# Kernel tuning notes

Measured on AMD Instinct MI355X. Metric: run time of the kernel, lower is better.

## Reference

```python
import jax, jax.numpy as jnp
import numpy as np

B, CIN, COUT, H, W, K, LATENT = 16, 512, 512, 64, 64, 3, 512
SQRT2 = float(np.sqrt(2.0))


def setup_inputs() -> dict:
    key = jax.random.key(0)
    ks = jax.random.split(key, 6)
    return {
        "x": jax.random.normal(ks[0], (B, CIN, H, W), jnp.float32),
        "latent": jax.random.normal(ks[1], (B, LATENT), jnp.float32),
        "noise": jax.random.normal(ks[2], (B, 1, H, W), jnp.float32),
        "affine_weight": jax.random.normal(ks[3], (CIN, LATENT), jnp.float32),
        "affine_bias": jnp.ones((CIN,), jnp.float32),
        "conv_weight": jax.random.normal(ks[4], (COUT, CIN, K, K), jnp.float32),
        "noise_weight": jax.random.normal(ks[5], (), jnp.float32),
        "bias": jnp.zeros((1, COUT, 1, 1), jnp.float32),
    }


def reference(x, latent, noise, affine_weight, affine_bias, conv_weight, noise_weight, bias):
    # NoiseInjection (applied before conv, as in the source)
    x = x + noise_weight * noise

    # AffineNetwork / EqualLinear: w * sqrt(1/in), leaky_relu(.,0.2)*sqrt(2)
    wmul = 1.0 / jnp.sqrt(jnp.float32(affine_weight.shape[1]))
    style = latent @ (affine_weight * wmul).T + affine_bias[None, :]
    style = jax.nn.leaky_relu(style, 0.2) * SQRT2  # [B, Cin]

    # Per-sample modulation (source overwrites the fan-in multiplier; raw weight used)
    w = conv_weight[None] * style[:, None, :, None, None]  # [B, Cout, Cin, kh, kw]
    demod = jax.lax.rsqrt(jnp.sum(w * w, axis=(2, 3, 4), keepdims=True) + 1e-8)
    w = w * demod

    def conv1(xi, wi):  # xi: [Cin,H,W], wi: [Cout,Cin,kh,kw]
        return jax.lax.conv_general_dilated(
            xi[None], wi, (1, 1), "SAME",
            dimension_numbers=("NCHW", "OIHW", "NCHW"))[0]

    out = jax.vmap(conv1)(x, w)  # [B, Cout, H, W]
    return jax.nn.leaky_relu(out + bias, 0.2) * SQRT2
```

## Files before the change

kernel.cpp:

```cpp
#include <hip/hip_runtime.h>

#define SQRT2F 1.41421356237309515f

typedef __attribute__((ext_vector_type(8))) short short8;
typedef __attribute__((ext_vector_type(4))) float floatx4;

static __device__ __forceinline__ unsigned short f2bf(float f) {
    unsigned int u = __float_as_uint(f);
    u += 0x7fffu + ((u >> 16) & 1u);
    return (unsigned short)(u >> 16);
}

static __device__ __forceinline__ void gl_lds16(const void* g, void* l) {
    __builtin_amdgcn_global_load_lds(
        (const __attribute__((address_space(1))) unsigned int*)g,
        (__attribute__((address_space(3))) unsigned int*)l, 16, 0, 0);
}

__global__ void style_kernel(const float* __restrict__ latent,
                             const float* __restrict__ aw,
                             const float* __restrict__ abias,
                             float* __restrict__ style) {
    const int b = blockIdx.x;
    const int t = threadIdx.x;
    const int c = blockIdx.y * 256 + t;
    __shared__ float lat[512];
    lat[t]       = latent[b * 512 + t];
    lat[t + 256] = latent[b * 512 + t + 256];
    __syncthreads();
    const float* row = aw + (size_t)c * 512;
    float s0 = 0.f, s1 = 0.f, s2 = 0.f, s3 = 0.f;
    #pragma unroll 4
    for (int k = 0; k < 512; k += 4) {
        floatx4 r = *(const floatx4*)(row + k);
        s0 += lat[k]     * r[0];
        s1 += lat[k + 1] * r[1];
        s2 += lat[k + 2] * r[2];
        s3 += lat[k + 3] * r[3];
    }
    float s = (s0 + s1) + (s2 + s3);
    s = s * 0.04419417382415922f + abias[c];
    s = (s > 0.f ? s : 0.2f * s) * SQRT2F;
    style[b * 512 + c] = s;
}

__global__ void wprep_kernel(const float* __restrict__ cw,
                             const float* __restrict__ style,
                             unsigned short* __restrict__ wbf,
                             float* __restrict__ demod) {
    const int co = blockIdx.x;
    const int t = threadIdx.x;
    __shared__ float raw[4608];
    __shared__ float sty2[8192];
    __shared__ float r2[512];
    const float* row = cw + (size_t)co * 4608;
    for (int i = t; i < 1152; i += 256)
        ((floatx4*)raw)[i] = ((const floatx4*)row)[i];
    for (int i = t; i < 2048; i += 256) {
        floatx4 v = ((const floatx4*)style)[i];
        ((floatx4*)sty2)[i] = v * v;
    }
    __syncthreads();
    for (int cin = t; cin < 512; cin += 256) {
        float s = 0.f;
        #pragma unroll
        for (int tap = 0; tap < 9; ++tap) { float v = raw[cin * 9 + tap]; s += v * v; }
        r2[cin] = s;
    }
    for (int j = t; j < 576; j += 256) {
        int st = j >> 2, chunk = j & 3;
        int slab = st / 9, tap = st - slab * 9;
        int cb = slab * 32 + chunk * 8;
        short8 o;
        #pragma unroll
        for (int k = 0; k < 8; ++k) o[k] = (short)f2bf(raw[(cb + k) * 9 + tap]);
        *(short8*)(wbf + ((size_t)st * 512 + co) * 32 + chunk * 8) = o;
    }
    __syncthreads();
    const int lane = t & 63, wv = t >> 6;
    #pragma unroll
    for (int bb = 0; bb < 4; ++bb) {
        int b = wv * 4 + bb;
        float s = 0.f;
        for (int cin = lane; cin < 512; cin += 64) s += r2[cin] * sty2[b * 512 + cin];
        #pragma unroll
        for (int off = 32; off > 0; off >>= 1) s += __shfl_down(s, off, 64);
        if (lane == 0) demod[b * 512 + co] = rsqrtf(s + 1e-8f);
    }
}

__global__ void xprep_kernel(const float* __restrict__ x,
                             const float* __restrict__ noise,
                             const float* __restrict__ nwp,
                             const float* __restrict__ style,
                             unsigned short* __restrict__ xp) {
    const int h = blockIdx.x, slab = blockIdx.y, b = blockIdx.z;
    const int t = threadIdx.x;
    __shared__ float tile[32][65];
    const float nw = nwp[0];
    const int w4 = (t & 15) * 4, rh = t >> 4;
    floatx4 nz = *(const floatx4*)(noise + (size_t)b * 4096 + h * 64 + w4);
    #pragma unroll
    for (int p = 0; p < 2; ++p) {
        int cl = p * 16 + rh;
        int cin = slab * 32 + cl;
        floatx4 v = *(const floatx4*)(x + ((size_t)(b * 512 + cin)) * 4096 + h * 64 + w4);
        float sv = style[b * 512 + cin];
        #pragma unroll
        for (int j = 0; j < 4; ++j) tile[cl][w4 + j] = (v[j] + nw * nz[j]) * sv;
    }
    __syncthreads();
    unsigned short* base = xp + ((size_t)(b * 16 + slab) * 4356) * 32;
    const int w2 = t >> 2, chunk = t & 3;
    short8 o;
    #pragma unroll
    for (int j = 0; j < 8; ++j) o[j] = (short)f2bf(tile[chunk * 8 + j][w2]);
    *(short8*)(base + ((size_t)(h + 1) * 66 + (w2 + 1)) * 32 + chunk * 8) = o;
    short8 z = {};
    if (t < 8) {
        int col = (t >> 2) * 65;
        *(short8*)(base + ((size_t)(h + 1) * 66 + col) * 32 + (t & 3) * 8) = z;
    }
    if (h == 0) {
        for (int i = t; i < 264; i += 256)
            *(short8*)(base + (size_t)(i >> 2) * 32 + (i & 3) * 8) = z;
    } else if (h == 63) {
        for (int i = t; i < 264; i += 256)
            *(short8*)(base + ((size_t)65 * 66 + (i >> 2)) * 32 + (i & 3) * 8) = z;
    }
}

__launch_bounds__(256, 2)
__global__ void conv_kernel(const unsigned short* __restrict__ xp,
                            const unsigned short* __restrict__ wbf,
                            const float* __restrict__ demod,
                            const float* __restrict__ bias,
                            float* __restrict__ out) {
    const int b   = blockIdx.z;
    const int co0 = blockIdx.y * 128;
    const int tr  = blockIdx.x >> 2, tc = blockIdx.x & 3;
    const int h0  = tr * 8, w0 = tc * 16;
    const int tid  = threadIdx.x;
    const int lane = tid & 63, wv = tid >> 6;
    const int wr = wv >> 1, wc = wv & 1;
    const int quad = lane >> 4, l16 = lane & 15;

    __shared__ __align__(16) unsigned short lds_x[2][6144];
    __shared__ __align__(16) unsigned short lds_w[2][12288];

    floatx4 acc[4][4] = {};

    int wso[6];
    #pragma unroll
    for (int it = 0; it < 6; ++it) {
        int co = (it * 64 + (tid >> 2)) & 127;
        int lchunk = (tid & 3) ^ ((co >> 1) & 3);
        wso[it] = (it >> 1) * 32768 + co * 64 + lchunk * 16;
    }
    int xo[3];
    #pragma unroll
    for (int it = 0; it < 3; ++it) {
        int pos = it * 64 + (tid >> 2);
        if (pos > 179) pos = 179;
        int r = pos / 18, c = pos - r * 18;
        int lchunk = (tid & 3) ^ ((pos >> 1) & 3);
        xo[it] = (r * 66 + c) * 64 + lchunk * 16;
    }
    const int wvb = wv * 1024;

    int a_off[4];
    #pragma unroll
    for (int mi = 0; mi < 4; ++mi) {
        int co = wr * 64 + mi * 16 + l16;
        a_off[mi] = co * 32 + (quad ^ ((co >> 1) & 3)) * 8;
    }
    int bo2[6][3];
    #pragma unroll
    for (int r = 0; r < 6; ++r)
        #pragma unroll
        for (int c = 0; c < 3; ++c) {
            int pos = (wc * 4 + r) * 18 + c + l16;
            bo2[r][c] = pos * 32 + (quad ^ ((pos >> 1) & 3)) * 8;
        }

    const char* xpb = (const char*)xp + ((size_t)b * 16 * 4356 + h0 * 66 + w0) * 64;
    const char* wb0 = (const char*)wbf + (size_t)co0 * 64;

    #pragma unroll
    for (int it = 0; it < 3; ++it)
        gl_lds16(xpb + xo[it], (char*)lds_x[0] + it * 4096 + wvb);
    #pragma unroll
    for (int it = 0; it < 6; ++it)
        gl_lds16(wb0 + wso[it], (char*)lds_w[0] + it * 4096 + wvb);

    for (int s = 0; s < 16; ++s) {
        short8 xf[6][3];
        #pragma unroll
        for (int g = 0; g < 3; ++g) {
            __syncthreads();
            if (g < 2) {
                const char* gw = wb0 + s * 294912 + (g + 1) * 98304;
                char* lw = (char*)lds_w[(s + g + 1) & 1];
                #pragma unroll
                for (int it = 0; it < 6; ++it)
                    gl_lds16(gw + wso[it], lw + it * 4096 + wvb);
            } else if (s < 15) {
                const char* gw = wb0 + (s + 1) * 294912;
                char* lw = (char*)lds_w[(s + 1) & 1];
                #pragma unroll
                for (int it = 0; it < 6; ++it)
                    gl_lds16(gw + wso[it], lw + it * 4096 + wvb);
            }
            if (g == 0 && s < 15) {
                const char* gx = xpb + (size_t)(s + 1) * 278784;
                char* lx = (char*)lds_x[(s + 1) & 1];
                #pragma unroll
                for (int it = 0; it < 3; ++it)
                    gl_lds16(gx + xo[it], lx + it * 4096 + wvb);
            }
            const unsigned short* wbuf = lds_w[(s + g) & 1];
            const unsigned short* xbuf = lds_x[s & 1];
            if (g == 0) {
                #pragma unroll
                for (int r = 0; r < 4; ++r)
                    #pragma unroll
                    for (int c = 0; c < 3; ++c)
                        xf[r][c] = *(const short8*)(xbuf + bo2[r][c]);
            } else {
                #pragma unroll
                for (int c = 0; c < 3; ++c)
                    xf[g + 3][c] = *(const short8*)(xbuf + bo2[g + 3][c]);
            }
            #pragma unroll
            for (int tl = 0; tl < 3; ++tl) {
                short8 a[4];
                #pragma unroll
                for (int mi = 0; mi < 4; ++mi)
                    a[mi] = *(const short8*)(wbuf + tl * 4096 + a_off[mi]);
                __builtin_amdgcn_s_setprio(1);
                #pragma unroll
                for (int mi = 0; mi < 4; ++mi)
                    #pragma unroll
                    for (int ni = 0; ni < 4; ++ni)
                        acc[mi][ni] = __builtin_amdgcn_mfma_f32_16x16x32_bf16(
                            a[mi], xf[ni + g][tl], acc[mi][ni], 0, 0, 0);
                __builtin_amdgcn_s_setprio(0);
            }
        }
    }

    const float* dmb = demod + b * 512;
    #pragma unroll
    for (int mi = 0; mi < 4; ++mi) {
        const int cob = co0 + wr * 64 + mi * 16 + quad * 4;
        float bv[4], dv[4];
        #pragma unroll
        for (int i = 0; i < 4; ++i) { bv[i] = bias[cob + i]; dv[i] = dmb[cob + i]; }
        #pragma unroll
        for (int ni = 0; ni < 4; ++ni) {
            const int gh = h0 + wc * 4 + ni;
            const int gw = w0 + l16;
            #pragma unroll
            for (int i = 0; i < 4; ++i) {
                float v = acc[mi][ni][i] * dv[i] + bv[i];
                v = (v > 0.f ? v : 0.2f * v) * SQRT2F;
                out[(((size_t)b * 512 + cob + i) * 64 + gh) * 64 + gw] = v;
            }
        }
    }
}

extern "C" void kernel_launch(void* const* d_in, const int* in_sizes, int n_in,
                              void* d_out, int out_size, void* d_ws, size_t ws_size,
                              hipStream_t stream) {
    const float* x      = (const float*)d_in[0];
    const float* latent = (const float*)d_in[1];
    const float* noise  = (const float*)d_in[2];
    const float* aw     = (const float*)d_in[3];
    const float* abias  = (const float*)d_in[4];
    const float* cw     = (const float*)d_in[5];
    const float* nwp    = (const float*)d_in[6];
    const float* bias   = (const float*)d_in[7];
    float* out = (float*)d_out;

    float* style         = (float*)d_ws;
    float* demod         = (float*)((char*)d_ws + 32768);
    unsigned short* wbf  = (unsigned short*)((char*)d_ws + 65536);
    unsigned short* xp   = (unsigned short*)((char*)d_ws + 65536 + 4718592);

    style_kernel<<<dim3(16, 2), dim3(256), 0, stream>>>(latent, aw, abias, style);
    wprep_kernel<<<dim3(512), dim3(256), 0, stream>>>(cw, style, wbf, demod);
    xprep_kernel<<<dim3(64, 16, 16), dim3(256), 0, stream>>>(x, noise, nwp, style, xp);
    conv_kernel<<<dim3(32, 4, 16), dim3(256), 0, stream>>>(xp, wbf, demod, bias, out);
}
```

Measured before the change: 501.0 us.

## Load conv weight fragments directly from global memory instead of staging in LDS

Weight A-fragments are now read straight from global memory into registers for each tap, and the LDS weight double-buffer and its async global-to-LDS copies are removed. Only the input tile is still staged through LDS, so there is one barrier per channel stage instead of three. This frees LDS and cuts barrier and LDS traffic. In exchange, each MFMA group now waits on global or L2 loads with little prefetch, and weights are re-read by both column waves.

```diff
diff --git a/kernel.cpp b/kernel.cpp
--- a/kernel.cpp
+++ b/kernel.cpp
@@ -146,17 +146,9 @@
     const int quad = lane >> 4, l16 = lane & 15;
 
     __shared__ __align__(16) unsigned short lds_x[2][6144];
-    __shared__ __align__(16) unsigned short lds_w[2][12288];
 
     floatx4 acc[4][4] = {};
 
-    int wso[6];
-    #pragma unroll
-    for (int it = 0; it < 6; ++it) {
-        int co = (it * 64 + (tid >> 2)) & 127;
-        int lchunk = (tid & 3) ^ ((co >> 1) & 3);
-        wso[it] = (it >> 1) * 32768 + co * 64 + lchunk * 16;
-    }
     int xo[3];
     #pragma unroll
     for (int it = 0; it < 3; ++it) {
@@ -168,12 +160,6 @@
     }
     const int wvb = wv * 1024;
 
-    int a_off[4];
-    #pragma unroll
-    for (int mi = 0; mi < 4; ++mi) {
-        int co = wr * 64 + mi * 16 + l16;
-        a_off[mi] = co * 32 + (quad ^ ((co >> 1) & 3)) * 8;
-    }
     int bo2[6][3];
     #pragma unroll
     for (int r = 0; r < 6; ++r)
@@ -184,42 +170,26 @@
         }
 
     const char* xpb = (const char*)xp + ((size_t)b * 16 * 4356 + h0 * 66 + w0) * 64;
-    const char* wb0 = (const char*)wbf + (size_t)co0 * 64;
+    const char* aB = (const char*)wbf + (size_t)(co0 + wr * 64 + l16) * 64 + quad * 16;
 
     #pragma unroll
     for (int it = 0; it < 3; ++it)
         gl_lds16(xpb + xo[it], (char*)lds_x[0] + it * 4096 + wvb);
-    #pragma unroll
-    for (int it = 0; it < 6; ++it)
-        gl_lds16(wb0 + wso[it], (char*)lds_w[0] + it * 4096 + wvb);
 
     for (int s = 0; s < 16; ++s) {
+        __syncthreads();
+        if (s < 15) {
+            const char* gx = xpb + (size_t)(s + 1) * 278784;
+            char* lx = (char*)lds_x[(s + 1) & 1];
+            #pragma unroll
+            for (int it = 0; it < 3; ++it)
+                gl_lds16(gx + xo[it], lx + it * 4096 + wvb);
+        }
+        const unsigned short* xbuf = lds_x[s & 1];
+        const char* aS = aB + (size_t)s * 294912;
         short8 xf[6][3];
         #pragma unroll
         for (int g = 0; g < 3; ++g) {
-            __syncthreads();
-            if (g < 2) {
-                const char* gw = wb0 + s * 294912 + (g + 1) * 98304;
-                char* lw = (char*)lds_w[(s + g + 1) & 1];
-                #pragma unroll
-                for (int it = 0; it < 6; ++it)
-                    gl_lds16(gw + wso[it], lw + it * 4096 + wvb);
-            } else if (s < 15) {
-                const char* gw = wb0 + (s + 1) * 294912;
-                char* lw = (char*)lds_w[(s + 1) & 1];
-                #pragma unroll
-                for (int it = 0; it < 6; ++it)
-                    gl_lds16(gw + wso[it], lw + it * 4096 + wvb);
-            }
-            if (g == 0 && s < 15) {
-                const char* gx = xpb + (size_t)(s + 1) * 278784;
-                char* lx = (char*)lds_x[(s + 1) & 1];
-                #pragma unroll
-                for (int it = 0; it < 3; ++it)
-                    gl_lds16(gx + xo[it], lx + it * 4096 + wvb);
-            }
-            const unsigned short* wbuf = lds_w[(s + g) & 1];
-            const unsigned short* xbuf = lds_x[s & 1];
             if (g == 0) {
                 #pragma unroll
                 for (int r = 0; r < 4; ++r)
@@ -236,7 +206,7 @@
                 short8 a[4];
                 #pragma unroll
                 for (int mi = 0; mi < 4; ++mi)
-                    a[mi] = *(const short8*)(wbuf + tl * 4096 + a_off[mi]);
+                    a[mi] = *(const short8*)(aS + (g * 3 + tl) * 32768 + mi * 1024);
                 __builtin_amdgcn_s_setprio(1);
                 #pragma unroll
                 for (int mi = 0; mi < 4; ++mi)
```

Result: slower. 559.1 us (+11.6%).
